# Performance work log

Measured on AMD Instinct MI355X. Metric: run time of the kernel, lower is better.

The kernel has to match this reference:

```python
import jax, jax.numpy as jnp
import numpy as np
from jax import lax

EPS = 1e-08


def setup_inputs() -> dict:
    key = jax.random.key(0)
    kX, kY, kXs, kW, kA, kB1, kB2 = jax.random.split(key, 7)
    P, D, K, M = 8192, 1024, 131072, 512
    return {
        "X": jax.random.normal(kX, (P, D), dtype=jnp.float32),
        "y": jax.random.normal(kY, (P,), dtype=jnp.float32),
        "X_star": jax.random.normal(kXs, (K, D), dtype=jnp.float32),
        "gamma": jnp.float32(0.001),
        "W": jax.random.normal(kW, (M, D), dtype=jnp.float32) * 0.01,
        "a": jax.random.normal(kA, (M,), dtype=jnp.float32) * 0.01,
        "b1": jax.random.normal(kB1, (M,), dtype=jnp.float32) * 0.01,
        "b2": jnp.float32(0.1),
        "L": 64,
    }


def reference(X, y, X_star, gamma, W, a, b1, b2, L):
    P, D = X.shape
    Sigma_hat = (X.T @ X) / P                      # (D, D)
    I = jnp.eye(D, dtype=X.dtype)
    M_mat = I - (gamma / L) * Sigma_hat            # (D, D)

    # S = sum_{l=0}^{L-1} M^l, built sequentially as in the original loop
    def step(carry, _):
        S, Mp = carry
        return (S + Mp, Mp @ M_mat), None

    (S, _), _ = lax.scan(step, (jnp.zeros_like(I), I), None, length=L)

    rep = gamma * (S @ (X.T @ y))                  # (D,)
    linear_pred = (X_star @ rep) / (L * P)         # (K,)

    rep_normalized = rep / (jnp.linalg.norm(rep) + EPS)
    phi = X_star * rep_normalized                  # (K, D) elementwise
    hidden = jax.nn.relu(phi @ W.T + b1)           # (K, m)
    mlp_correction = hidden @ a                    # (K,)
    return linear_pred + mlp_correction + b2
```

## Files before the change

kernel.cpp:

```cpp
#include <hip/hip_runtime.h>
#include <hip/hip_bf16.h>
#include <stdint.h>

#define D_DIM 1024
#define P_ROWS 8192
#define K_ROWS 131072
#define M_DIM 512
#define L_STEPS 64
#define BM 128

typedef short bf16x8_t __attribute__((ext_vector_type(8)));
typedef float f32x4_t __attribute__((ext_vector_type(4)));

typedef const __attribute__((address_space(1))) void* gas_t;
typedef __attribute__((address_space(3))) void* las_t;

__device__ __forceinline__ uint32_t f2bf(float f) {
  union { float f; uint32_t u; } c; c.f = f;
  const uint32_t u = c.u;
  return (u + 0x7FFFu + ((u >> 16) & 1u)) >> 16;
}

__global__ void xty_kernel(const float* __restrict__ X, const float* __restrict__ y,
                           float* __restrict__ v) {
  const int d0 = threadIdx.x * 4;
  float a0 = 0.f, a1 = 0.f, a2 = 0.f, a3 = 0.f;
  for (int i = blockIdx.x; i < P_ROWS; i += gridDim.x) {
    const float s = y[i];
    const float4 x = *reinterpret_cast<const float4*>(X + (size_t)i * D_DIM + d0);
    a0 += s * x.x; a1 += s * x.y; a2 += s * x.z; a3 += s * x.w;
  }
  atomicAdd(v + d0 + 0, a0);
  atomicAdd(v + d0 + 1, a1);
  atomicAdd(v + d0 + 2, a2);
  atomicAdd(v + d0 + 3, a3);
}

__global__ void xtxw_kernel(const float* __restrict__ X, const float* __restrict__ win,
                            float* __restrict__ wout) {
  __shared__ float red[4][D_DIM];
  const int lane = threadIdx.x & 63;
  const int wave = threadIdx.x >> 6;
  const int gw = blockIdx.x * 4 + wave;
  const int nw = gridDim.x * 4;
  float wv[16], acc[16];
#pragma unroll
  for (int q = 0; q < 4; ++q) {
    const float4 tv = *reinterpret_cast<const float4*>(win + q * 256 + lane * 4);
    wv[q*4+0] = tv.x; wv[q*4+1] = tv.y; wv[q*4+2] = tv.z; wv[q*4+3] = tv.w;
  }
#pragma unroll
  for (int j = 0; j < 16; ++j) acc[j] = 0.f;
  for (int i = gw; i < P_ROWS; i += nw) {
    const float* xr = X + (size_t)i * D_DIM;
    float xv[16];
    float dot = 0.f;
#pragma unroll
    for (int q = 0; q < 4; ++q) {
      const float4 tv = *reinterpret_cast<const float4*>(xr + q * 256 + lane * 4);
      xv[q*4+0] = tv.x; xv[q*4+1] = tv.y; xv[q*4+2] = tv.z; xv[q*4+3] = tv.w;
      dot += tv.x * wv[q*4+0] + tv.y * wv[q*4+1] + tv.z * wv[q*4+2] + tv.w * wv[q*4+3];
    }
#pragma unroll
    for (int m = 1; m < 64; m <<= 1) dot += __shfl_xor(dot, m);
#pragma unroll
    for (int j = 0; j < 16; ++j) acc[j] += dot * xv[j];
  }
#pragma unroll
  for (int q = 0; q < 4; ++q) {
    float4 tv;
    tv.x = acc[q*4+0]; tv.y = acc[q*4+1]; tv.z = acc[q*4+2]; tv.w = acc[q*4+3];
    *reinterpret_cast<float4*>(&red[wave][q * 256 + lane * 4]) = tv;
  }
  __syncthreads();
  const int d0 = threadIdx.x * 4;
#pragma unroll
  for (int j = 0; j < 4; ++j)
    atomicAdd(wout + d0 + j, red[0][d0+j] + red[1][d0+j] + red[2][d0+j] + red[3][d0+j]);
}

__global__ void combine_kernel(const float* __restrict__ v, const float* __restrict__ u1,
                               const float* __restrict__ u2, const float* __restrict__ gamma_p,
                               float* __restrict__ rep_lin, float* __restrict__ repn) {
  __shared__ float sred[4];
  const float gamma = *gamma_p;
  const float eps = gamma / (float)L_STEPS;
  const float c1 = 2016.0f * eps / (float)P_ROWS;
  const float c2 = 41664.0f * eps * eps / ((float)P_ROWS * (float)P_ROWS);
  const int d0 = threadIdx.x * 4;
  float r[4];
  float ss = 0.f;
#pragma unroll
  for (int j = 0; j < 4; ++j) {
    const float val = gamma * ((float)L_STEPS * v[d0+j] - c1 * u1[d0+j] + c2 * u2[d0+j]);
    r[j] = val;
    ss += val * val;
  }
#pragma unroll
  for (int m = 1; m < 64; m <<= 1) ss += __shfl_xor(ss, m);
  if ((threadIdx.x & 63) == 0) sred[threadIdx.x >> 6] = ss;
  __syncthreads();
  const float norm = sqrtf(sred[0] + sred[1] + sred[2] + sred[3]);
  const float inv_norm = 1.0f / (norm + 1e-8f);
  const float lin_s = 1.0f / ((float)L_STEPS * (float)P_ROWS);
#pragma unroll
  for (int j = 0; j < 4; ++j) {
    rep_lin[d0+j] = r[j] * lin_s;
    repn[d0+j]    = r[j] * inv_norm;
  }
}

__global__ void wn_frag_kernel(const float* __restrict__ W, const float* __restrict__ repn,
                               ushort* __restrict__ WnF) {
  const int gid = blockIdx.x * 256 + threadIdx.x;
  const int l = gid & 63;
  const int f = (gid >> 6) & 31;
  const int s = gid >> 11;
  const int m = f * 16 + (l & 15);
  const int d0 = s * 32 + ((l >> 4) << 3);
  const float4 w0 = *reinterpret_cast<const float4*>(W + (size_t)m * D_DIM + d0);
  const float4 w1 = *reinterpret_cast<const float4*>(W + (size_t)m * D_DIM + d0 + 4);
  const float4 r0 = *reinterpret_cast<const float4*>(repn + d0);
  const float4 r1 = *reinterpret_cast<const float4*>(repn + d0 + 4);
  uint32_t p0 = f2bf(w0.x*r0.x) | (f2bf(w0.y*r0.y) << 16);
  uint32_t p1 = f2bf(w0.z*r0.z) | (f2bf(w0.w*r0.w) << 16);
  uint32_t p2 = f2bf(w1.x*r1.x) | (f2bf(w1.y*r1.y) << 16);
  uint32_t p3 = f2bf(w1.z*r1.z) | (f2bf(w1.w*r1.w) << 16);
  uint4 o; o.x = p0; o.y = p1; o.z = p2; o.w = p3;
  *reinterpret_cast<uint4*>(WnF + (size_t)gid * 8) = o;
}

__global__ __launch_bounds__(512, 2)
void fused_kernel(const float* __restrict__ Xs, const ushort* __restrict__ WnF,
                  const float* __restrict__ rep_lin, const float* __restrict__ b1,
                  const float* __restrict__ aw, const float* __restrict__ b2p,
                  float* __restrict__ out) {
  __shared__ float  Af[3 * 4096];
  __shared__ ushort Bh[2 * 16384];
  __shared__ float  repl[D_DIM];
  __shared__ float  mlp_acc[BM];
  __shared__ float  lin_acc[BM];

  const int t = threadIdx.x;
  const int lane = t & 63;
  const int wid = t >> 6;
  const int wm = wid >> 2;
  const int wn = wid & 3;
  const int fr = lane & 15;
  const int kg = lane >> 4;
  const size_t blockRow = (size_t)blockIdx.x * BM;

  char* AfB = (char*)Af;
  char* BhB = (char*)Bh;
  const char* WnB = (const char*)WnF;
  const char* replB = (const char*)repl;

  const char* gA0 = (const char*)Xs
      + (blockRow + (size_t)wid * 16 + (lane >> 3)) * (D_DIM * 4)
      + (size_t)(((lane & 7) ^ (lane >> 3)) * 16);
  const char* gA1 = gA0 + (size_t)8 * (D_DIM * 4);

  const int aoff0 = (wm * 64 + fr) * 128 + (((kg * 2)     ^ (lane & 7)) * 16);
  const int aoff1 = (wm * 64 + fr) * 128 + (((kg * 2 + 1) ^ (lane & 7)) * 16);
  const int rowL = t >> 2;
  const int cL = (t & 3) * 2;
  const int loffA0 = rowL * 128 + ((cL      ^ (rowL & 7)) * 16);
  const int loffA1 = rowL * 128 + (((cL | 1) ^ (rowL & 7)) * 16);

  f32x4_t acc[4][8];
#pragma unroll
  for (int mi = 0; mi < 4; ++mi)
#pragma unroll
    for (int ni = 0; ni < 8; ++ni)
      acc[mi][ni] = f32x4_t{0.f, 0.f, 0.f, 0.f};
  float linreg = 0.f;

  auto stageB = [&](int sn) {
    const char* src = WnB + (size_t)sn * 32768 + (size_t)wid * 4096 + (size_t)lane * 16;
    char* dst = BhB + (size_t)(sn & 1) * 32768 + (size_t)wid * 4096;
#pragma unroll
    for (int j = 0; j < 4; ++j)
      __builtin_amdgcn_global_load_lds((gas_t)(src + j * 1024), (las_t)(dst + j * 1024), 16, 0, 0);
  };
  auto stageA = [&](int s2) {
    char* dst = AfB + (size_t)(s2 % 3) * 16384 + (size_t)wid * 2048;
    __builtin_amdgcn_global_load_lds((gas_t)(gA0 + (size_t)s2 * 128), (las_t)dst, 16, 0, 0);
    __builtin_amdgcn_global_load_lds((gas_t)(gA1 + (size_t)s2 * 128), (las_t)(dst + 1024), 16, 0, 0);
  };
  auto compute = [&](int s) {
    const char* Ab = AfB + (size_t)(s % 3) * 16384;
    const char* Bb = BhB + (size_t)(s & 1) * 32768;
    bf16x8_t bfr[8];
#pragma unroll
    for (int ni = 0; ni < 8; ++ni)
      bfr[ni] = *reinterpret_cast<const bf16x8_t*>(Bb + wn * 8192 + ni * 1024 + lane * 16);
    bf16x8_t afr[4];
#pragma unroll
    for (int mi = 0; mi < 4; ++mi) {
      f32x4_t v0 = *reinterpret_cast<const f32x4_t*>(Ab + aoff0 + mi * 2048);
      f32x4_t v1 = *reinterpret_cast<const f32x4_t*>(Ab + aoff1 + mi * 2048);
      uint32_t p0, p1, p2, p3;
      asm("v_cvt_pk_bf16_f32 %0, %1, %2" : "=v"(p0) : "v"(v0[0]), "v"(v0[1]));
      asm("v_cvt_pk_bf16_f32 %0, %1, %2" : "=v"(p1) : "v"(v0[2]), "v"(v0[3]));
      asm("v_cvt_pk_bf16_f32 %0, %1, %2" : "=v"(p2) : "v"(v1[0]), "v"(v1[1]));
      asm("v_cvt_pk_bf16_f32 %0, %1, %2" : "=v"(p3) : "v"(v1[2]), "v"(v1[3]));
      union { uint32_t u[4]; bf16x8_t h; } cv;
      cv.u[0] = p0; cv.u[1] = p1; cv.u[2] = p2; cv.u[3] = p3;
      afr[mi] = cv.h;
    }
#pragma unroll
    for (int mi = 0; mi < 4; ++mi)
#pragma unroll
      for (int ni = 0; ni < 8; ++ni)
        acc[mi][ni] = __builtin_amdgcn_mfma_f32_16x16x32_bf16(afr[mi], bfr[ni], acc[mi][ni], 0, 0, 0);
    f32x4_t la0 = *reinterpret_cast<const f32x4_t*>(Ab + loffA0);
    f32x4_t la1 = *reinterpret_cast<const f32x4_t*>(Ab + loffA1);
    f32x4_t lr0 = *reinterpret_cast<const f32x4_t*>(replB + s * 128 + (t & 3) * 32);
    f32x4_t lr1 = *reinterpret_cast<const f32x4_t*>(replB + s * 128 + (t & 3) * 32 + 16);
    linreg += la0[0]*lr0[0] + la0[1]*lr0[1] + la0[2]*lr0[2] + la0[3]*lr0[3]
            + la1[0]*lr1[0] + la1[1]*lr1[1] + la1[2]*lr1[2] + la1[3]*lr1[3];
  };

  stageB(0);
  stageA(0);
  stageA(1);
  if (t < BM) mlp_acc[t] = 0.f;
  repl[t] = rep_lin[t];
  repl[t + 512] = rep_lin[t + 512];
  asm volatile("s_waitcnt vmcnt(0)" ::: "memory");
  __syncthreads();

  for (int s = 0; s < 30; ++s) {
    stageB(s + 1);
    stageA(s + 2);
    __builtin_amdgcn_sched_barrier(0);
    compute(s);
    asm volatile("s_waitcnt vmcnt(2)" ::: "memory");
    __builtin_amdgcn_sched_barrier(0);
    __builtin_amdgcn_s_barrier();
  }
  stageB(31);
  __builtin_amdgcn_sched_barrier(0);
  compute(30);
  asm volatile("s_waitcnt vmcnt(0)" ::: "memory");
  __builtin_amdgcn_sched_barrier(0);
  __builtin_amdgcn_s_barrier();
  compute(31);

  linreg += __shfl_xor(linreg, 1);
  linreg += __shfl_xor(linreg, 2);
  if ((t & 3) == 0) lin_acc[rowL] = linreg;

  float b1r[8], ar[8];
#pragma unroll
  for (int ni = 0; ni < 8; ++ni) {
    const int c = wn * 128 + ni * 16 + fr;
    b1r[ni] = b1[c];
    ar[ni]  = aw[c];
  }
#pragma unroll
  for (int mi = 0; mi < 4; ++mi) {
#pragma unroll
    for (int r = 0; r < 4; ++r) {
      float sum = 0.f;
#pragma unroll
      for (int ni = 0; ni < 8; ++ni) {
        const float h = acc[mi][ni][r] + b1r[ni];
        sum += fmaxf(h, 0.f) * ar[ni];
      }
      sum += __shfl_xor(sum, 1);
      sum += __shfl_xor(sum, 2);
      sum += __shfl_xor(sum, 4);
      sum += __shfl_xor(sum, 8);
      if (fr == 0) {
        const int row = wm * 64 + mi * 16 + kg * 4 + r;
        atomicAdd(&mlp_acc[row], sum);
      }
    }
  }
  __syncthreads();
  if (t < BM)
    out[blockRow + t] = lin_acc[t] + mlp_acc[t] + b2p[0];
}

extern "C" void kernel_launch(void* const* d_in, const int* in_sizes, int n_in,
                              void* d_out, int out_size, void* d_ws, size_t ws_size,
                              hipStream_t stream) {
  const float* X     = (const float*)d_in[0];
  const float* y     = (const float*)d_in[1];
  const float* Xs    = (const float*)d_in[2];
  const float* gamma = (const float*)d_in[3];
  const float* W     = (const float*)d_in[4];
  const float* a     = (const float*)d_in[5];
  const float* b1    = (const float*)d_in[6];
  const float* b2    = (const float*)d_in[7];
  float* out = (float*)d_out;

  char* ws = (char*)d_ws;
  float*  v       = (float*)(ws + 0);
  float*  u1      = (float*)(ws + 4096);
  float*  u2      = (float*)(ws + 8192);
  float*  rep_lin = (float*)(ws + 12288);
  float*  repn    = (float*)(ws + 16384);
  ushort* WnF     = (ushort*)(ws + 20480);

  hipMemsetAsync(ws, 0, 3 * 4096, stream);
  hipLaunchKernelGGL(xty_kernel,     dim3(256), dim3(256), 0, stream, X, y, v);
  hipLaunchKernelGGL(xtxw_kernel,    dim3(256), dim3(256), 0, stream, X, v, u1);
  hipLaunchKernelGGL(xtxw_kernel,    dim3(256), dim3(256), 0, stream, X, u1, u2);
  hipLaunchKernelGGL(combine_kernel, dim3(1),   dim3(256), 0, stream, v, u1, u2, gamma, rep_lin, repn);
  hipLaunchKernelGGL(wn_frag_kernel, dim3(256), dim3(256), 0, stream, W, repn, WnF);
  hipLaunchKernelGGL(fused_kernel,   dim3(K_ROWS / BM), dim3(512), 0, stream,
                     Xs, WnF, rep_lin, b1, a, b2, out);
}
```

Baseline: 342.6 us.

## Convert X_star to bf16 in registers before LDS and triple-buffer weights

```diff
diff --git a/kernel.cpp b/kernel.cpp
--- a/kernel.cpp
+++ b/kernel.cpp
@@ -19,6 +19,9 @@
   union { float f; uint32_t u; } c; c.f = f;
   const uint32_t u = c.u;
   return (u + 0x7FFFu + ((u >> 16) & 1u)) >> 16;
+}
+__device__ __forceinline__ uint32_t pack2(float lo, float hi) {
+  return f2bf(lo) | (f2bf(hi) << 16);
 }
 
 __global__ void xty_kernel(const float* __restrict__ X, const float* __restrict__ y,
@@ -122,11 +125,11 @@
   const float4 w1 = *reinterpret_cast<const float4*>(W + (size_t)m * D_DIM + d0 + 4);
   const float4 r0 = *reinterpret_cast<const float4*>(repn + d0);
   const float4 r1 = *reinterpret_cast<const float4*>(repn + d0 + 4);
-  uint32_t p0 = f2bf(w0.x*r0.x) | (f2bf(w0.y*r0.y) << 16);
-  uint32_t p1 = f2bf(w0.z*r0.z) | (f2bf(w0.w*r0.w) << 16);
-  uint32_t p2 = f2bf(w1.x*r1.x) | (f2bf(w1.y*r1.y) << 16);
-  uint32_t p3 = f2bf(w1.z*r1.z) | (f2bf(w1.w*r1.w) << 16);
-  uint4 o; o.x = p0; o.y = p1; o.z = p2; o.w = p3;
+  uint4 o;
+  o.x = f2bf(w0.x*r0.x) | (f2bf(w0.y*r0.y) << 16);
+  o.y = f2bf(w0.z*r0.z) | (f2bf(w0.w*r0.w) << 16);
+  o.z = f2bf(w1.x*r1.x) | (f2bf(w1.y*r1.y) << 16);
+  o.w = f2bf(w1.z*r1.z) | (f2bf(w1.w*r1.w) << 16);
   *reinterpret_cast<uint4*>(WnF + (size_t)gid * 8) = o;
 }
 
@@ -135,11 +138,10 @@
                   const float* __restrict__ rep_lin, const float* __restrict__ b1,
                   const float* __restrict__ aw, const float* __restrict__ b2p,
                   float* __restrict__ out) {
-  __shared__ float  Af[3 * 4096];
-  __shared__ ushort Bh[2 * 16384];
-  __shared__ float  repl[D_DIM];
-  __shared__ float  mlp_acc[BM];
-  __shared__ float  lin_acc[BM];
+  __shared__ __align__(16) ushort Bh[3 * 16384];
+  __shared__ __align__(16) ushort Ah[2 * 4096];
+  __shared__ float mlp_acc[BM];
+  __shared__ float lin_acc[BM];
 
   const int t = threadIdx.x;
   const int lane = t & 63;
@@ -148,108 +150,130 @@
   const int wn = wid & 3;
   const int fr = lane & 15;
   const int kg = lane >> 4;
+  const int R  = t >> 2;
+  const int cq = t & 3;
   const size_t blockRow = (size_t)blockIdx.x * BM;
 
-  char* AfB = (char*)Af;
   char* BhB = (char*)Bh;
+  char* AhB = (char*)Ah;
   const char* WnB = (const char*)WnF;
-  const char* replB = (const char*)repl;
-
-  const char* gA0 = (const char*)Xs
-      + (blockRow + (size_t)wid * 16 + (lane >> 3)) * (D_DIM * 4)
-      + (size_t)(((lane & 7) ^ (lane >> 3)) * 16);
-  const char* gA1 = gA0 + (size_t)8 * (D_DIM * 4);
-
-  const int aoff0 = (wm * 64 + fr) * 128 + (((kg * 2)     ^ (lane & 7)) * 16);
-  const int aoff1 = (wm * 64 + fr) * 128 + (((kg * 2 + 1) ^ (lane & 7)) * 16);
-  const int rowL = t >> 2;
-  const int cL = (t & 3) * 2;
-  const int loffA0 = rowL * 128 + ((cL      ^ (rowL & 7)) * 16);
-  const int loffA1 = rowL * 128 + (((cL | 1) ^ (rowL & 7)) * 16);
-
-  f32x4_t acc[4][8];
-#pragma unroll
-  for (int mi = 0; mi < 4; ++mi)
-#pragma unroll
-    for (int ni = 0; ni < 8; ++ni)
-      acc[mi][ni] = f32x4_t{0.f, 0.f, 0.f, 0.f};
-  float linreg = 0.f;
+  const char* gA = (const char*)Xs + (blockRow + (size_t)R) * (D_DIM * 4) + (size_t)cq * 32;
+  const char* gR = (const char*)rep_lin + cq * 32;
+
+  const int aw_off  = (R >> 4) * 1024 + (((cq << 4) | (R & 15)) * 16);
+  const int ar_base = (wm * 4) * 1024 + lane * 16;
+  const int br_base = wn * 8192 + lane * 16;
 
   auto stageB = [&](int sn) {
     const char* src = WnB + (size_t)sn * 32768 + (size_t)wid * 4096 + (size_t)lane * 16;
-    char* dst = BhB + (size_t)(sn & 1) * 32768 + (size_t)wid * 4096;
+    char* dst = BhB + (size_t)(sn % 3) * 32768 + (size_t)wid * 4096;
 #pragma unroll
     for (int j = 0; j < 4; ++j)
       __builtin_amdgcn_global_load_lds((gas_t)(src + j * 1024), (las_t)(dst + j * 1024), 16, 0, 0);
   };
-  auto stageA = [&](int s2) {
-    char* dst = AfB + (size_t)(s2 % 3) * 16384 + (size_t)wid * 2048;
-    __builtin_amdgcn_global_load_lds((gas_t)(gA0 + (size_t)s2 * 128), (las_t)dst, 16, 0, 0);
-    __builtin_amdgcn_global_load_lds((gas_t)(gA1 + (size_t)s2 * 128), (las_t)(dst + 1024), 16, 0, 0);
+
+  float linreg = 0.f;
+  auto stageA_math = [&](int sn, const float4& a0, const float4& a1,
+                         const float4& r0, const float4& r1) {
+    linreg += a0.x*r0.x + a0.y*r0.y + a0.z*r0.z + a0.w*r0.w
+            + a1.x*r1.x + a1.y*r1.y + a1.z*r1.z + a1.w*r1.w;
+    uint4 p;
+    p.x = pack2(a0.x, a0.y); p.y = pack2(a0.z, a0.w);
+    p.z = pack2(a1.x, a1.y); p.w = pack2(a1.z, a1.w);
+    *reinterpret_cast<uint4*>(AhB + (sn & 1) * 8192 + aw_off) = p;
   };
-  auto compute = [&](int s) {
-    const char* Ab = AfB + (size_t)(s % 3) * 16384;
-    const char* Bb = BhB + (size_t)(s & 1) * 32768;
-    bf16x8_t bfr[8];
+
+  f32x4_t acc[4][8];
+#pragma unroll
+  for (int mi = 0; mi < 4; ++mi)
 #pragma unroll
     for (int ni = 0; ni < 8; ++ni)
-      bfr[ni] = *reinterpret_cast<const bf16x8_t*>(Bb + wn * 8192 + ni * 1024 + lane * 16);
-    bf16x8_t afr[4];
-#pragma unroll
-    for (int mi = 0; mi < 4; ++mi) {
-      f32x4_t v0 = *reinterpret_cast<const f32x4_t*>(Ab + aoff0 + mi * 2048);
-      f32x4_t v1 = *reinterpret_cast<const f32x4_t*>(Ab + aoff1 + mi * 2048);
-      uint32_t p0, p1, p2, p3;
-      asm("v_cvt_pk_bf16_f32 %0, %1, %2" : "=v"(p0) : "v"(v0[0]), "v"(v0[1]));
-      asm("v_cvt_pk_bf16_f32 %0, %1, %2" : "=v"(p1) : "v"(v0[2]), "v"(v0[3]));
-      asm("v_cvt_pk_bf16_f32 %0, %1, %2" : "=v"(p2) : "v"(v1[0]), "v"(v1[1]));
-      asm("v_cvt_pk_bf16_f32 %0, %1, %2" : "=v"(p3) : "v"(v1[2]), "v"(v1[3]));
-      union { uint32_t u[4]; bf16x8_t h; } cv;
-      cv.u[0] = p0; cv.u[1] = p1; cv.u[2] = p2; cv.u[3] = p3;
-      afr[mi] = cv.h;
-    }
+      acc[mi][ni] = f32x4_t{0.f, 0.f, 0.f, 0.f};
+
+  {
+    const float4 a0 = *reinterpret_cast<const float4*>(gA);
+    const float4 a1 = *reinterpret_cast<const float4*>(gA + 16);
+    const float4 r0 = *reinterpret_cast<const float4*>(gR);
+    const float4 r1 = *reinterpret_cast<const float4*>(gR + 16);
+    __builtin_amdgcn_sched_barrier(0);
+    stageB(0);
+    stageB(1);
+    __builtin_amdgcn_sched_barrier(0);
+    if (t < BM) mlp_acc[t] = 0.f;
+    stageA_math(0, a0, a1, r0, r1);
+    asm volatile("s_waitcnt vmcnt(4) lgkmcnt(0)" ::: "memory");
+    __builtin_amdgcn_s_barrier();
+  }
+
+  for (int s = 0; s < 30; ++s) {
+    const int rb = (s % 3) * 32768;
+    const int ab = (s & 1) * 8192;
+    const float4 a0 = *reinterpret_cast<const float4*>(gA + (s + 1) * 128);
+    const float4 a1 = *reinterpret_cast<const float4*>(gA + (s + 1) * 128 + 16);
+    const float4 r0 = *reinterpret_cast<const float4*>(gR + (s + 1) * 128);
+    const float4 r1 = *reinterpret_cast<const float4*>(gR + (s + 1) * 128 + 16);
+    bf16x8_t bfr[8], afr[4];
+#pragma unroll
+    for (int ni = 0; ni < 8; ++ni)
+      bfr[ni] = *reinterpret_cast<const bf16x8_t*>(BhB + rb + br_base + ni * 1024);
+#pragma unroll
+    for (int mi = 0; mi < 4; ++mi)
+      afr[mi] = *reinterpret_cast<const bf16x8_t*>(AhB + ab + ar_base + mi * 1024);
+    __builtin_amdgcn_sched_barrier(0);
+    stageB(s + 2);
+    __builtin_amdgcn_sched_barrier(0);
+    __builtin_amdgcn_s_setprio(1);
 #pragma unroll
     for (int mi = 0; mi < 4; ++mi)
 #pragma unroll
       for (int ni = 0; ni < 8; ++ni)
         acc[mi][ni] = __builtin_amdgcn_mfma_f32_16x16x32_bf16(afr[mi], bfr[ni], acc[mi][ni], 0, 0, 0);
-    f32x4_t la0 = *reinterpret_cast<const f32x4_t*>(Ab + loffA0);
-    f32x4_t la1 = *reinterpret_cast<const f32x4_t*>(Ab + loffA1);
-    f32x4_t lr0 = *reinterpret_cast<const f32x4_t*>(replB + s * 128 + (t & 3) * 32);
-    f32x4_t lr1 = *reinterpret_cast<const f32x4_t*>(replB + s * 128 + (t & 3) * 32 + 16);
-    linreg += la0[0]*lr0[0] + la0[1]*lr0[1] + la0[2]*lr0[2] + la0[3]*lr0[3]
-            + la1[0]*lr1[0] + la1[1]*lr1[1] + la1[2]*lr1[2] + la1[3]*lr1[3];
-  };
-
-  stageB(0);
-  stageA(0);
-  stageA(1);
-  if (t < BM) mlp_acc[t] = 0.f;
-  repl[t] = rep_lin[t];
-  repl[t + 512] = rep_lin[t + 512];
-  asm volatile("s_waitcnt vmcnt(0)" ::: "memory");
-  __syncthreads();
-
-  for (int s = 0; s < 30; ++s) {
-    stageB(s + 1);
-    stageA(s + 2);
-    __builtin_amdgcn_sched_barrier(0);
-    compute(s);
-    asm volatile("s_waitcnt vmcnt(2)" ::: "memory");
-    __builtin_amdgcn_sched_barrier(0);
+    __builtin_amdgcn_s_setprio(0);
+    stageA_math(s + 1, a0, a1, r0, r1);
+    asm volatile("s_waitcnt vmcnt(4) lgkmcnt(0)" ::: "memory");
     __builtin_amdgcn_s_barrier();
   }
-  stageB(31);
-  __builtin_amdgcn_sched_barrier(0);
-  compute(30);
-  asm volatile("s_waitcnt vmcnt(0)" ::: "memory");
-  __builtin_amdgcn_sched_barrier(0);
-  __builtin_amdgcn_s_barrier();
-  compute(31);
+
+  {
+    const int s = 30;
+    const float4 a0 = *reinterpret_cast<const float4*>(gA + 31 * 128);
+    const float4 a1 = *reinterpret_cast<const float4*>(gA + 31 * 128 + 16);
+    const float4 r0 = *reinterpret_cast<const float4*>(gR + 31 * 128);
+    const float4 r1 = *reinterpret_cast<const float4*>(gR + 31 * 128 + 16);
+    bf16x8_t bfr[8], afr[4];
+#pragma unroll
+    for (int ni = 0; ni < 8; ++ni)
+      bfr[ni] = *reinterpret_cast<const bf16x8_t*>(BhB + (s % 3) * 32768 + br_base + ni * 1024);
+#pragma unroll
+    for (int mi = 0; mi < 4; ++mi)
+      afr[mi] = *reinterpret_cast<const bf16x8_t*>(AhB + (s & 1) * 8192 + ar_base + mi * 1024);
+#pragma unroll
+    for (int mi = 0; mi < 4; ++mi)
+#pragma unroll
+      for (int ni = 0; ni < 8; ++ni)
+        acc[mi][ni] = __builtin_amdgcn_mfma_f32_16x16x32_bf16(afr[mi], bfr[ni], acc[mi][ni], 0, 0, 0);
+    stageA_math(31, a0, a1, r0, r1);
+    asm volatile("s_waitcnt vmcnt(0) lgkmcnt(0)" ::: "memory");
+    __builtin_amdgcn_s_barrier();
+  }
+  {
+    bf16x8_t bfr[8], afr[4];
+#pragma unroll
+    for (int ni = 0; ni < 8; ++ni)
+      bfr[ni] = *reinterpret_cast<const bf16x8_t*>(BhB + (31 % 3) * 32768 + br_base + ni * 1024);
+#pragma unroll
+    for (int mi = 0; mi < 4; ++mi)
+      afr[mi] = *reinterpret_cast<const bf16x8_t*>(AhB + 8192 + ar_base + mi * 1024);
+#pragma unroll
+    for (int mi = 0; mi < 4; ++mi)
+#pragma unroll
+      for (int ni = 0; ni < 8; ++ni)
+        acc[mi][ni] = __builtin_amdgcn_mfma_f32_16x16x32_bf16(afr[mi], bfr[ni], acc[mi][ni], 0, 0, 0);
+  }
 
   linreg += __shfl_xor(linreg, 1);
   linreg += __shfl_xor(linreg, 2);
-  if ((t & 3) == 0) lin_acc[rowL] = linreg;
+  if (cq == 0) lin_acc[R] = linreg;
 
   float b1r[8], ar[8];
 #pragma unroll
```

Result: faster. 325.5 us (-5.0%).
